# Optimization experiments

Measured on AMD Instinct MI355X. Metric: run time of the kernel, lower is better.

## Reference

```python
import jax, jax.numpy as jnp
import numpy as np

B, T, D_IN = 32, 32, 128
N_SLOTS, M_LEN = 512, 64
NUM_SHIFT, NUM_READ, NUM_WRITE = 3, 4, 1
CTRL_DIM = 256
READ_HEAD_LEN = 3 + M_LEN + NUM_SHIFT            # k, beta, g, s, gamma
WRITE_HEAD_LEN = READ_HEAD_LEN + 2 * M_LEN       # + erase, add vectors
INSTR_DIM = NUM_READ * READ_HEAD_LEN + NUM_WRITE * WRITE_HEAD_LEN


def setup_inputs() -> dict:
    key = jax.random.key(0)
    ks = jax.random.split(key, 4)
    def glorot(k, shape):
        lim = np.sqrt(6.0 / (shape[0] + shape[1])).astype(np.float32)
        return jax.random.uniform(k, shape, jnp.float32, -lim, lim)
    return {
        "x": jax.random.normal(ks[0], (B, T, D_IN), jnp.float32),
        "Wc": glorot(ks[1], (D_IN + NUM_READ * M_LEN, CTRL_DIM)),
        "bc": jnp.zeros((CTRL_DIM,), jnp.float32),
        "heads_kernel": glorot(ks[2], (CTRL_DIM, INSTR_DIM)),
        "heads_bias": jnp.zeros((INSTR_DIM,), jnp.float32),
    }


def _parse_heads(h):
    # h: (B, H, 3 + M + S) -> k, beta, g, s, gamma per _get_weight_vector
    k = h[..., :M_LEN]
    b = jnp.exp(h[..., M_LEN])
    g = jax.nn.sigmoid(h[..., M_LEN + 1])
    s = jax.nn.softmax(h[..., M_LEN + 2:M_LEN + 2 + NUM_SHIFT], axis=-1)
    t = jax.nn.softplus(h[..., M_LEN + 2 + NUM_SHIFT]) + 1.0
    return k, b, g, s, t


def _address(Mem, w_prev, k, b, g, s, t):
    # Mem:(B,N,M) k:(B,H,M) w_prev:(B,H,N) b,g,t:(B,H) s:(B,H,S)
    eps = 1e-8
    Mn = jnp.linalg.norm(Mem, axis=-1)                       # (B,N)
    kn = jnp.linalg.norm(k, axis=-1)                         # (B,H)
    sim = jnp.einsum('bhm,bnm->bhn', k, Mem) / (kn[..., None] * Mn[:, None, :] + eps)
    wc = jax.nn.softmax(b[..., None] * sim, axis=-1)         # content
    wg = g[..., None] * wc + (1.0 - g[..., None]) * w_prev   # gate
    half = NUM_SHIFT // 2                                    # circular shift conv
    wsh = sum(s[..., i:i + 1] * jnp.roll(wg, i - half, axis=-1) for i in range(NUM_SHIFT))
    wt = wsh ** t[..., None]                                 # sharpen
    return wt / (jnp.sum(wt, axis=-1, keepdims=True) + eps)


def _ntm_forward(x, Wc, bc, heads_kernel, heads_bias):
    def step(carry, x_t):
        r, rw, ww, Mem = carry
        # dense controller on [x_t, old read vectors]
        ctrl_in = jnp.concatenate([x_t, r.reshape(B, -1)], axis=-1)
        h = jnp.tanh(ctrl_in @ Wc + bc)                      # controller_out == instr
        instr = h @ heads_kernel + heads_bias                # (B, INSTR_DIM)
        rh = instr[:, :NUM_READ * READ_HEAD_LEN].reshape(B, NUM_READ, READ_HEAD_LEN)
        wh = instr[:, NUM_READ * READ_HEAD_LEN:].reshape(B, NUM_WRITE, WRITE_HEAD_LEN)
        rw_n = _address(Mem, rw, *_parse_heads(rh))
        ww_n = _address(Mem, ww, *_parse_heads(wh[..., :READ_HEAD_LEN]))
        e = wh[..., READ_HEAD_LEN:READ_HEAD_LEN + M_LEN]     # raw erase (no sigmoid, as in source)
        a = wh[..., READ_HEAD_LEN + M_LEN:]                  # raw add
        # erase all heads, then add all heads (source loops erase first)
        Mem = Mem * jnp.prod(1.0 - ww_n[..., :, None] * e[..., None, :], axis=1)
        Mem = Mem + jnp.einsum('bwn,bwm->bnm', ww_n, a)
        r_n = jnp.einsum('bnm,brn->brm', Mem, rw_n)          # read
        return (r_n, rw_n, ww_n, Mem), h

    init = (jnp.zeros((B, NUM_READ, M_LEN), jnp.float32),
            jnp.zeros((B, NUM_READ, N_SLOTS), jnp.float32),
            jnp.zeros((B, NUM_WRITE, N_SLOTS), jnp.float32),
            jnp.zeros((B, N_SLOTS, M_LEN), jnp.float32))
    _, outs = jax.lax.scan(step, init, jnp.swapaxes(x, 0, 1))  # time-major
    return outs[-1]  # return_sequences=False -> last controller output (B, CTRL_DIM)


def reference(x, Wc, bc, heads_kernel, heads_bias):
    return _ntm_forward(x, Wc, bc, heads_kernel, heads_bias)
```

## Files before the change

kernel.cpp:

```cpp
#include <hip/hip_runtime.h>
#include <math.h>

#define BB 32
#define TT 32
#define D_INX 128
#define NSLOT 512
#define MLEN 64
#define NREAD 4
#define NHEAD 5
#define CDIM 256
#define IDIM 478
#define RHL 70
#define NT 512

#define HKB_OFF 196608

struct SMem {
    float mem[NSLOT * MLEN];
    float wprev[NHEAD * NSLOT];
    float mn[NSLOT];
    float ctrl[384];
    float h[CDIM];
    float instr[480];
    float k[NHEAD * MLEN];
    float e[MLEN];
    float a[MLEN];
    float u[2560];
};

__device__ __forceinline__ unsigned short f2bf(float f) {
    unsigned u = __float_as_uint(f);
    return (unsigned short)((u + 0x7fffu + ((u >> 16) & 1u)) >> 16);
}

__global__ void pack_kernel(const float* __restrict__ Wc, const float* __restrict__ Hk,
                            unsigned short* __restrict__ wctb, unsigned short* __restrict__ hkb)
{
    int idx = blockIdx.x * 256 + threadIdx.x;
    if (idx < 384 * 256) {
        int i = idx >> 8, col = idx & 255;
        wctb[((i >> 3) * 256 + col) * 8 + (i & 7)] = f2bf(Wc[idx]);
    }
    if (idx < 256 * 478) {
        int i = idx / 478, col = idx - i * 478;
        hkb[((i >> 3) * 478 + col) * 8 + (i & 7)] = f2bf(Hk[idx]);
    }
}

#define BF8_DOT(wv, c0, c1, c2, c3, acc) do {                                   \
    unsigned _u0 = __float_as_uint((wv).x), _u1 = __float_as_uint((wv).y);      \
    unsigned _u2 = __float_as_uint((wv).z), _u3 = __float_as_uint((wv).w);      \
    acc += __uint_as_float(_u0 << 16) * (c0).x + __uint_as_float(_u0 & 0xffff0000u) * (c0).y; \
    acc += __uint_as_float(_u1 << 16) * (c1).x + __uint_as_float(_u1 & 0xffff0000u) * (c1).y; \
    acc += __uint_as_float(_u2 << 16) * (c2).x + __uint_as_float(_u2 & 0xffff0000u) * (c2).y; \
    acc += __uint_as_float(_u3 << 16) * (c3).x + __uint_as_float(_u3 & 0xffff0000u) * (c3).y; \
} while (0)

__global__ __launch_bounds__(NT, 2)
void ntm_kernel(const float* __restrict__ x,
                const float* __restrict__ bc,
                const float* __restrict__ hb,
                const unsigned short* __restrict__ wctb,
                const unsigned short* __restrict__ hkb,
                float* __restrict__ out)
{
    extern __shared__ float smem_f[];
    SMem* sc = (SMem*)smem_f;

    const int b    = blockIdx.x;
    const int tid  = threadIdx.x;
    const int lane = tid & 63;
    const int wave = tid >> 6;

    const float bcv = (tid < CDIM) ? bc[tid] : 0.f;
    const float hbv = (tid < IDIM) ? hb[tid] : 0.f;

    {
        float4 z4 = make_float4(0.f, 0.f, 0.f, 0.f);
        float4* m4 = (float4*)sc->mem;
        for (int i = tid; i < NSLOT * MLEN / 4; i += NT) m4[i] = z4;
        for (int i = tid; i < NHEAD * NSLOT; i += NT) sc->wprev[i] = 0.f;
        sc->mn[tid] = 0.f;
        if (tid < 384) sc->ctrl[tid] = (tid < D_INX) ? x[(size_t)b * TT * D_INX + tid] : 0.f;
    }
    __syncthreads();

    for (int t = 0; t < TT; ++t) {
        {
            int col = tid & 255, kb = tid >> 8;
            const float4* wq = (const float4*)wctb + kb * 24 * 256 + col;
            const float2* c2 = (const float2*)sc->ctrl + kb * 96;
            float acc = 0.f;
#pragma unroll
            for (int cc = 0; cc < 24; ++cc) {
                float4 wv = wq[cc * 256];
                float2 x0 = c2[cc * 4], x1 = c2[cc * 4 + 1], x2 = c2[cc * 4 + 2], x3 = c2[cc * 4 + 3];
                BF8_DOT(wv, x0, x1, x2, x3, acc);
            }
            sc->u[kb * 256 + col] = acc;
        }
        __syncthreads();

        if (tid < CDIM) {
            float hv = tanhf(bcv + sc->u[tid] + sc->u[256 + tid]);
            sc->h[tid] = hv;
            if (t == TT - 1) out[(size_t)b * CDIM + tid] = hv;
        } else if (tid < 384 && t + 1 < TT) {
            sc->ctrl[tid - 256] = x[((size_t)b * TT + t + 1) * D_INX + (tid - 256)];
        }
        if (t == TT - 1) break;
        __syncthreads();

        if (tid < IDIM) {
            const float4* wq = (const float4*)hkb + tid;
            const float2* h2 = (const float2*)sc->h;
            float acc = hbv;
#pragma unroll
            for (int c = 0; c < 32; ++c) {
                float4 wv = wq[c * 478];
                float2 x0 = h2[c * 4], x1 = h2[c * 4 + 1], x2 = h2[c * 4 + 2], x3 = h2[c * 4 + 3];
                BF8_DOT(wv, x0, x1, x2, x3, acc);
            }
            sc->instr[tid] = acc;
            if (tid < 350) {
                int hh = (tid * 937) >> 16;
                int m = tid - hh * RHL;
                if (m < MLEN) sc->k[hh * MLEN + m] = acc;
            } else if (tid < 414) {
                sc->e[tid - 350] = acc;
            } else {
                sc->a[tid - 414] = acc;
            }
        }
        __syncthreads();

        {
            int n = tid, nx = n & 15;
            const float4* m4 = (const float4*)sc->mem + n * 16;
            const float4* k4 = (const float4*)sc->k;
            float d0 = 0.f, d1 = 0.f, d2 = 0.f, d3 = 0.f, d4 = 0.f;
#pragma unroll
            for (int j = 0; j < 16; ++j) {
                float4 mv = m4[j ^ nx];
                float4 k0 = k4[j], k1 = k4[16 + j], k2 = k4[32 + j], k3 = k4[48 + j], kw = k4[64 + j];
                d0 += mv.x * k0.x + mv.y * k0.y + mv.z * k0.z + mv.w * k0.w;
                d1 += mv.x * k1.x + mv.y * k1.y + mv.z * k1.z + mv.w * k1.w;
                d2 += mv.x * k2.x + mv.y * k2.y + mv.z * k2.z + mv.w * k2.w;
                d3 += mv.x * k3.x + mv.y * k3.y + mv.z * k3.z + mv.w * k3.w;
                d4 += mv.x * kw.x + mv.y * kw.y + mv.z * kw.z + mv.w * kw.w;
            }
            sc->u[n] = d0; sc->u[512 + n] = d1; sc->u[1024 + n] = d2;
            sc->u[1536 + n] = d3; sc->u[2048 + n] = d4;
        }
        __syncthreads();

        if (wave < NHEAD) {
            const int h = wave;
            const float* ins = sc->instr + h * RHL;
            float kv = ins[lane];
            float sq = kv * kv;
#pragma unroll
            for (int off = 32; off; off >>= 1) sq += __shfl_xor(sq, off);
            float kn = sqrtf(sq);
            float beta = __expf(ins[64]);
            float g = 1.f / (1.f + __expf(-ins[65]));
            float v0 = ins[66], v1 = ins[67], v2 = ins[68];
            float mx3 = fmaxf(v0, fmaxf(v1, v2));
            float e0 = __expf(v0 - mx3), e1 = __expf(v1 - mx3), e2 = __expf(v2 - mx3);
            float inv3 = 1.f / (e0 + e1 + e2);
            float s0 = e0 * inv3, s1 = e1 * inv3, s2 = e2 * inv3;
            float tv = ins[69];
            float tp = fmaxf(tv, 0.f) + log1pf(__expf(-fabsf(tv))) + 1.f;

            float uu[8];
#pragma unroll
            for (int j = 0; j < 8; ++j) {
                int slot = j * 64 + lane;
                float d = sc->u[h * NSLOT + slot];
                uu[j] = beta * d / (kn * sc->mn[slot] + 1e-8f);
            }
            float m = uu[0];
#pragma unroll
            for (int j = 1; j < 8; ++j) m = fmaxf(m, uu[j]);
#pragma unroll
            for (int off = 32; off; off >>= 1) m = fmaxf(m, __shfl_xor(m, off));
            float ev[8]; float Z = 0.f;
#pragma unroll
            for (int j = 0; j < 8; ++j) { ev[j] = __expf(uu[j] - m); Z += ev[j]; }
#pragma unroll
            for (int off = 32; off; off >>= 1) Z += __shfl_xor(Z, off);
            float invZ = 1.f / Z;
            float wg[8];
#pragma unroll
            for (int j = 0; j < 8; ++j) {
                int slot = j * 64 + lane;
                wg[j] = g * ev[j] * invZ + (1.f - g) * sc->wprev[h * NSLOT + slot];
            }
            int lm = (lane + 63) & 63, lp = (lane + 1) & 63;
            float rm[8], rp[8], b63[8], b0[8];
#pragma unroll
            for (int j = 0; j < 8; ++j) {
                rm[j]  = __shfl(wg[j], lm);
                rp[j]  = __shfl(wg[j], lp);
                b63[j] = __shfl(wg[j], 63);
                b0[j]  = __shfl(wg[j], 0);
            }
            if (lane == 0) {
#pragma unroll
                for (int j = 0; j < 8; ++j) rm[j] = b63[(j + 7) & 7];
            }
            if (lane == 63) {
#pragma unroll
                for (int j = 0; j < 8; ++j) rp[j] = b0[(j + 1) & 7];
            }
            float wt[8]; float S = 0.f;
#pragma unroll
            for (int j = 0; j < 8; ++j) {
                float wsh = s0 * rp[j] + s1 * wg[j] + s2 * rm[j];
                wt[j] = __builtin_amdgcn_exp2f(tp * __builtin_amdgcn_logf(wsh));
                S += wt[j];
            }
#pragma unroll
            for (int off = 32; off; off >>= 1) S += __shfl_xor(S, off);
            float invS = 1.f / (S + 1e-8f);
#pragma unroll
            for (int j = 0; j < 8; ++j)
                sc->wprev[h * NSLOT + j * 64 + lane] = wt[j] * invS;
        }
        __syncthreads();

        {
            int n = tid, nx = n & 15;
            float4* m4 = (float4*)sc->mem + n * 16;
            const float4* e4 = (const float4*)sc->e;
            const float4* a4 = (const float4*)sc->a;
            float wv = sc->wprev[4 * NSLOT + n];
            float nsq = 0.f;
#pragma unroll
            for (int j = 0; j < 16; ++j) {
                float4 mv = m4[j ^ nx];
                float4 ev = e4[j], av = a4[j];
                mv.x = mv.x * (1.f - wv * ev.x) + wv * av.x;
                mv.y = mv.y * (1.f - wv * ev.y) + wv * av.y;
                mv.z = mv.z * (1.f - wv * ev.z) + wv * av.z;
                mv.w = mv.w * (1.f - wv * ev.w) + wv * av.w;
                nsq += mv.x * mv.x + mv.y * mv.y + mv.z * mv.z + mv.w * mv.w;
                m4[j ^ nx] = mv;
            }
            sc->mn[n] = sqrtf(nsq);
        }
        __syncthreads();

        {
            int rg = lane >> 4, j = lane & 15;
            int base = wave * 64;
            float4 ac[4];
#pragma unroll
            for (int hh = 0; hh < 4; ++hh) ac[hh] = make_float4(0.f, 0.f, 0.f, 0.f);
#pragma unroll
            for (int i = 0; i < 16; ++i) {
                int n = base + 4 * i + rg;
                float4 mv = ((const float4*)sc->mem)[n * 16 + (j ^ (n & 15))];
                float w0 = sc->wprev[n], w1 = sc->wprev[512 + n];
                float w2 = sc->wprev[1024 + n], w3 = sc->wprev[1536 + n];
                ac[0].x += w0 * mv.x; ac[0].y += w0 * mv.y; ac[0].z += w0 * mv.z; ac[0].w += w0 * mv.w;
                ac[1].x += w1 * mv.x; ac[1].y += w1 * mv.y; ac[1].z += w1 * mv.z; ac[1].w += w1 * mv.w;
                ac[2].x += w2 * mv.x; ac[2].y += w2 * mv.y; ac[2].z += w2 * mv.z; ac[2].w += w2 * mv.w;
                ac[3].x += w3 * mv.x; ac[3].y += w3 * mv.y; ac[3].z += w3 * mv.z; ac[3].w += w3 * mv.w;
            }
            float* af = (float*)ac;
#pragma unroll
            for (int q = 0; q < 16; ++q) {
                af[q] += __shfl_xor(af[q], 16);
                af[q] += __shfl_xor(af[q], 32);
            }
            if (rg == 0) {
                float4* rp = (float4*)(sc->u + wave * 256);
                rp[0 * 16 + j] = ac[0];
                rp[1 * 16 + j] = ac[1];
                rp[2 * 16 + j] = ac[2];
                rp[3 * 16 + j] = ac[3];
            }
        }
        __syncthreads();

        if (tid < 256) {
            float s = 0.f;
#pragma unroll
            for (int w = 0; w < 8; ++w) s += sc->u[w * 256 + tid];
            sc->ctrl[128 + tid] = s;
        }
        __syncthreads();
    }
}

extern "C" void kernel_launch(void* const* d_in, const int* in_sizes, int n_in,
                              void* d_out, int out_size, void* d_ws, size_t ws_size,
                              hipStream_t stream) {
    const float* x  = (const float*)d_in[0];
    const float* Wc = (const float*)d_in[1];
    const float* bc = (const float*)d_in[2];
    const float* Hk = (const float*)d_in[3];
    const float* hb = (const float*)d_in[4];
    float* out = (float*)d_out;

    unsigned short* wctb = (unsigned short*)d_ws;
    unsigned short* hkb  = (unsigned short*)((char*)d_ws + HKB_OFF);

    static_assert(sizeof(SMem) <= 163840, "LDS overflow");
    (void)hipFuncSetAttribute((const void*)ntm_kernel,
                              hipFuncAttributeMaxDynamicSharedMemorySize,
                              (int)sizeof(SMem));

    hipLaunchKernelGGL(pack_kernel, dim3(478), dim3(256), 0, stream, Wc, Hk, wctb, hkb);
    hipLaunchKernelGGL(ntm_kernel, dim3(BB), dim3(NT), sizeof(SMem), stream,
                       x, bc, hb, wctb, hkb, out);
}
```

Before: 905.4 us.

## Fuse similarity dots into addressing, prefetch head weights, interleave read weights

Moves the memory-key dot products into the per-head addressing waves, so one phase and one barrier go away. The cost is that only 5 of 8 waves do that work, each covering 8 slots. Head-kernel weights are half-prefetched before the barrier, and the remaining half is loaded ahead of the dot product to hide global latency. Read weights are stored interleaved so the read phase can load them as one float4. Shared-memory operands are loaded as float4, and tanhf is replaced by an exp2-based formula. Register pressure rises from the 16-entry weight and key arrays, which could lower occupancy.

```diff
diff --git a/kernel.cpp b/kernel.cpp
--- a/kernel.cpp
+++ b/kernel.cpp
@@ -17,7 +17,8 @@
 
 struct SMem {
     float mem[NSLOT * MLEN];
-    float wprev[NHEAD * NSLOT];
+    float wread4[NSLOT * 4];
+    float wwrite[NSLOT];
     float mn[NSLOT];
     float ctrl[384];
     float h[CDIM];
@@ -47,13 +48,13 @@
     }
 }
 
-#define BF8_DOT(wv, c0, c1, c2, c3, acc) do {                                   \
+#define BF8_DOT4(wv, cA, cB, acc) do {                                          \
     unsigned _u0 = __float_as_uint((wv).x), _u1 = __float_as_uint((wv).y);      \
     unsigned _u2 = __float_as_uint((wv).z), _u3 = __float_as_uint((wv).w);      \
-    acc += __uint_as_float(_u0 << 16) * (c0).x + __uint_as_float(_u0 & 0xffff0000u) * (c0).y; \
-    acc += __uint_as_float(_u1 << 16) * (c1).x + __uint_as_float(_u1 & 0xffff0000u) * (c1).y; \
-    acc += __uint_as_float(_u2 << 16) * (c2).x + __uint_as_float(_u2 & 0xffff0000u) * (c2).y; \
-    acc += __uint_as_float(_u3 << 16) * (c3).x + __uint_as_float(_u3 & 0xffff0000u) * (c3).y; \
+    acc += __uint_as_float(_u0 << 16) * (cA).x + __uint_as_float(_u0 & 0xffff0000u) * (cA).y; \
+    acc += __uint_as_float(_u1 << 16) * (cA).z + __uint_as_float(_u1 & 0xffff0000u) * (cA).w; \
+    acc += __uint_as_float(_u2 << 16) * (cB).x + __uint_as_float(_u2 & 0xffff0000u) * (cB).y; \
+    acc += __uint_as_float(_u3 << 16) * (cB).z + __uint_as_float(_u3 & 0xffff0000u) * (cB).w; \
 } while (0)
 
 __global__ __launch_bounds__(NT, 2)
@@ -79,7 +80,8 @@
         float4 z4 = make_float4(0.f, 0.f, 0.f, 0.f);
         float4* m4 = (float4*)sc->mem;
         for (int i = tid; i < NSLOT * MLEN / 4; i += NT) m4[i] = z4;
-        for (int i = tid; i < NHEAD * NSLOT; i += NT) sc->wprev[i] = 0.f;
+        ((float4*)sc->wread4)[tid] = z4;
+        sc->wwrite[tid] = 0.f;
         sc->mn[tid] = 0.f;
         if (tid < 384) sc->ctrl[tid] = (tid < D_INX) ? x[(size_t)b * TT * D_INX + tid] : 0.f;
     }
@@ -89,20 +91,30 @@
         {
             int col = tid & 255, kb = tid >> 8;
             const float4* wq = (const float4*)wctb + kb * 24 * 256 + col;
-            const float2* c2 = (const float2*)sc->ctrl + kb * 96;
+            const float4* c4 = (const float4*)sc->ctrl + kb * 48;
             float acc = 0.f;
 #pragma unroll
             for (int cc = 0; cc < 24; ++cc) {
                 float4 wv = wq[cc * 256];
-                float2 x0 = c2[cc * 4], x1 = c2[cc * 4 + 1], x2 = c2[cc * 4 + 2], x3 = c2[cc * 4 + 3];
-                BF8_DOT(wv, x0, x1, x2, x3, acc);
+                float4 cA = c4[cc * 2], cB = c4[cc * 2 + 1];
+                BF8_DOT4(wv, cA, cB, acc);
             }
             sc->u[kb * 256 + col] = acc;
         }
+        float4 wA[16];
+        if (tid < IDIM) {
+            const float4* wq = (const float4*)hkb + tid;
+#pragma unroll
+            for (int c = 0; c < 16; ++c) wA[c] = wq[c * IDIM];
+        }
         __syncthreads();
 
         if (tid < CDIM) {
-            float hv = tanhf(bcv + sc->u[tid] + sc->u[256 + tid]);
+            float v = bcv + sc->u[tid] + sc->u[256 + tid];
+            float av = fabsf(v);
+            float ex = __builtin_amdgcn_exp2f(av * 2.8853900817779268f);
+            float r1 = 1.f - 2.f / (ex + 1.f);
+            float hv = (v < 0.f) ? -r1 : r1;
             sc->h[tid] = hv;
             if (t == TT - 1) out[(size_t)b * CDIM + tid] = hv;
         } else if (tid < 384 && t + 1 < TT) {
@@ -113,13 +125,20 @@
 
         if (tid < IDIM) {
             const float4* wq = (const float4*)hkb + tid;
-            const float2* h2 = (const float2*)sc->h;
+            float4 wB[16];
+#pragma unroll
+            for (int c = 0; c < 16; ++c) wB[c] = wq[(16 + c) * IDIM];
+            const float4* h4 = (const float4*)sc->h;
             float acc = hbv;
 #pragma unroll
-            for (int c = 0; c < 32; ++c) {
-                float4 wv = wq[c * 478];
-                float2 x0 = h2[c * 4], x1 = h2[c * 4 + 1], x2 = h2[c * 4 + 2], x3 = h2[c * 4 + 3];
-                BF8_DOT(wv, x0, x1, x2, x3, acc);
+            for (int c = 0; c < 16; ++c) {
+                float4 cA = h4[c * 2], cB = h4[c * 2 + 1];
+                BF8_DOT4(wA[c], cA, cB, acc);
+            }
+#pragma unroll
+            for (int c = 0; c < 16; ++c) {
+                float4 cA = h4[32 + c * 2], cB = h4[33 + c * 2];
+                BF8_DOT4(wB[c], cA, cB, acc);
             }
             sc->instr[tid] = acc;
             if (tid < 350) {
@@ -134,34 +153,34 @@
         }
         __syncthreads();
 
-        {
-            int n = tid, nx = n & 15;
-            const float4* m4 = (const float4*)sc->mem + n * 16;
-            const float4* k4 = (const float4*)sc->k;
-            float d0 = 0.f, d1 = 0.f, d2 = 0.f, d3 = 0.f, d4 = 0.f;
-#pragma unroll
-            for (int j = 0; j < 16; ++j) {
-                float4 mv = m4[j ^ nx];
-                float4 k0 = k4[j], k1 = k4[16 + j], k2 = k4[32 + j], k3 = k4[48 + j], kw = k4[64 + j];
-                d0 += mv.x * k0.x + mv.y * k0.y + mv.z * k0.z + mv.w * k0.w;
-                d1 += mv.x * k1.x + mv.y * k1.y + mv.z * k1.z + mv.w * k1.w;
-                d2 += mv.x * k2.x + mv.y * k2.y + mv.z * k2.z + mv.w * k2.w;
-                d3 += mv.x * k3.x + mv.y * k3.y + mv.z * k3.z + mv.w * k3.w;
-                d4 += mv.x * kw.x + mv.y * kw.y + mv.z * kw.z + mv.w * kw.w;
-            }
-            sc->u[n] = d0; sc->u[512 + n] = d1; sc->u[1024 + n] = d2;
-            sc->u[1536 + n] = d3; sc->u[2048 + n] = d4;
-        }
-        __syncthreads();
-
         if (wave < NHEAD) {
             const int h = wave;
+            const float4* k4 = (const float4*)sc->k + h * 16;
+            float4 kk[16];
+#pragma unroll
+            for (int q = 0; q < 16; ++q) kk[q] = k4[q];
+            float sq = 0.f;
+#pragma unroll
+            for (int q = 0; q < 16; ++q)
+                sq += kk[q].x * kk[q].x + kk[q].y * kk[q].y + kk[q].z * kk[q].z + kk[q].w * kk[q].w;
+            float kn = sqrtf(sq);
+
+            float dots[8], mnv[8];
+#pragma unroll
+            for (int j = 0; j < 8; ++j) {
+                int n = j * 64 + lane, nx = n & 15;
+                const float4* m4 = (const float4*)sc->mem + n * 16;
+                float d = 0.f;
+#pragma unroll
+                for (int q = 0; q < 16; ++q) {
+                    float4 mv = m4[q ^ nx];
+                    d += mv.x * kk[q].x + mv.y * kk[q].y + mv.z * kk[q].z + mv.w * kk[q].w;
+                }
+                dots[j] = d;
+                mnv[j] = sc->mn[n];
+            }
+
             const float* ins = sc->instr + h * RHL;
-            float kv = ins[lane];
-            float sq = kv * kv;
-#pragma unroll
-            for (int off = 32; off; off >>= 1) sq += __shfl_xor(sq, off);
-            float kn = sqrtf(sq);
             float beta = __expf(ins[64]);
             float g = 1.f / (1.f + __expf(-ins[65]));
             float v0 = ins[66], v1 = ins[67], v2 = ins[68];
@@ -174,11 +193,9 @@
 
             float uu[8];
 #pragma unroll
-            for (int j = 0; j < 8; ++j) {
-                int slot = j * 64 + lane;
-                float d = sc->u[h * NSLOT + slot];
-                uu[j] = beta * d / (kn * sc->mn[slot] + 1e-8f);
-            }
+            for (int j = 0; j < 8; ++j)
+                uu[j] = beta * dots[j] / (kn * mnv[j] + 1e-8f);
+
             float m = uu[0];
 #pragma unroll
             for (int j = 1; j < 8; ++j) m = fmaxf(m, uu[j]);
@@ -190,11 +207,13 @@
 #pragma unroll
             for (int off = 32; off; off >>= 1) Z += __shfl_xor(Z, off);
             float invZ = 1.f / Z;
+
             float wg[8];
 #pragma unroll
             for (int j = 0; j < 8; ++j) {
-                int slot = j * 64 + lane;
-                wg[j] = g * ev[j] * invZ + (1.f - g) * sc->wprev[h * NSLOT + slot];
+                int n = j * 64 + lane;
+                float wp = (h < 4) ? sc->wread4[n * 4 + h] : sc->wwrite[n];
+                wg[j] = g * ev[j] * invZ + (1.f - g) * wp;
             }
             int lm = (lane + 63) & 63, lp = (lane + 1) & 63;
             float rm[8], rp[8], b63[8], b0[8];
@@ -223,9 +242,15 @@
 #pragma unroll
             for (int off = 32; off; off >>= 1) S += __shfl_xor(S, off);
             float invS = 1.f / (S + 1e-8f);
-#pragma unroll
-            for (int j = 0; j < 8; ++j)
-                sc->wprev[h * NSLOT + j * 64 + lane] = wt[j] * invS;
+            if (h < 4) {
+#pragma unroll
+                for (int j = 0; j < 8; ++j)
+                    sc->wread4[(j * 64 + lane) * 4 + h] = wt[j] * invS;
+            } else {
+#pragma unroll
+                for (int j = 0; j < 8; ++j)
+                    sc->wwrite[j * 64 + lane] = wt[j] * invS;
+            }
         }
         __syncthreads();
 
@@ -234,7 +259,7 @@
             float4* m4 = (float4*)sc->mem + n * 16;
             const float4* e4 = (const float4*)sc->e;
             const float4* a4 = (const float4*)sc->a;
-            float wv = sc->wprev[4 * NSLOT + n];
+            float wv = sc->wwrite[n];
             float nsq = 0.f;
 #pragma unroll
             for (int j = 0; j < 16; ++j) {
@@ -261,12 +286,11 @@
             for (int i = 0; i < 16; ++i) {
                 int n = base + 4 * i + rg;
                 float4 mv = ((const float4*)sc->mem)[n * 16 + (j ^ (n & 15))];
-                float w0 = sc->wprev[n], w1 = sc->wprev[512 + n];
-                float w2 = sc->wprev[1024 + n], w3 = sc->wprev[1536 + n];
-                ac[0].x += w0 * mv.x; ac[0].y += w0 * mv.y; ac[0].z += w0 * mv.z; ac[0].w += w0 * mv.w;
-                ac[1].x += w1 * mv.x; ac[1].y += w1 * mv.y; ac[1].z += w1 * mv.z; ac[1].w += w1 * mv.w;
-                ac[2].x += w2 * mv.x; ac[2].y += w2 * mv.y; ac[2].z += w2 * mv.z; ac[2].w += w2 * mv.w;
-                ac[3].x += w3 * mv.x; ac[3].y += w3 * mv.y; ac[3].z += w3 * mv.z; ac[3].w += w3 * mv.w;
+                float4 wv = ((const float4*)sc->wread4)[n];
+                ac[0].x += wv.x * mv.x; ac[0].y += wv.x * mv.y; ac[0].z += wv.x * mv.z; ac[0].w += wv.x * mv.w;
+                ac[1].x += wv.y * mv.x; ac[1].y += wv.y * mv.y; ac[1].z += wv.y * mv.z; ac[1].w += wv.y * mv.w;
+                ac[2].x += wv.z * mv.x; ac[2].y += wv.z * mv.y; ac[2].z += wv.z * mv.z; ac[2].w += wv.z * mv.w;
+                ac[3].x += wv.w * mv.x; ac[3].y += wv.w * mv.y; ac[3].z += wv.w * mv.z; ac[3].w += wv.w * mv.w;
             }
             float* af = (float*)ac;
 #pragma unroll
```

Measured after the change: 1.284 ms. +41.8%, slower.
